# Kernel tuning notes

Hardware: AMD Instinct MI355X
Metric: run time of the kernel (lower is better)

## Reference

```python
import jax, jax.numpy as jnp
import numpy as np

N, M, D, K = 32768, 8192, 384, 9


def setup_inputs() -> dict:
    key = jax.random.key(0)
    k1, k2 = jax.random.split(key)
    return {
        "embedding": jax.random.normal(k1, (N, D), dtype=jnp.float32),
        "memory_bank": jax.random.normal(k2, (M, D), dtype=jnp.float32),
        "n_neighbors": K,
    }


def reference(embedding, memory_bank, n_neighbors):
    x_norm = jnp.sum(embedding * embedding, axis=-1, keepdims=True)      # [N, 1]
    y_norm = jnp.sum(memory_bank * memory_bank, axis=-1, keepdims=True)  # [M, 1]
    d2 = x_norm - 2.0 * jnp.matmul(embedding, memory_bank.T) + y_norm.T  # [N, M]
    dist = jnp.sqrt(jnp.maximum(d2, 0.0))
    # topk smallest along dim 1 (patch_scores, indices discarded)
    neg_top, _ = jax.lax.top_k(-dist, n_neighbors)
    patch_scores = -neg_top  # [N, K], ascending distances
    return patch_scores
```

## Files before the change

kernel.cpp:

```cpp
#include <hip/hip_runtime.h>
#include <hip/hip_bf16.h>

#define N_ROWS 32768
#define M_ROWS 8192
#define D_DIM  384
#define K_NB   9
#define BN     64
#define MHALF  (M_ROWS / 2)
#define TILES  (MHALF / BN)
#define KP     6

#define QRANGE 2048.0f
#define QSCALE (1.0f / 2048.0f)
#define QSTEPF (QRANGE / 65535.0f)
#define M2S    (-2.0f * QSCALE)
#define BIGF   3.0e38f

typedef long i64;
typedef __attribute__((ext_vector_type(2))) long i64x2;
typedef __attribute__((ext_vector_type(4))) float f32x4;
typedef __attribute__((ext_vector_type(2))) unsigned short u16x2;

__global__ __launch_bounds__(256) void FAPM_prep8(
    const float* __restrict__ emb, const float* __restrict__ mem,
    unsigned* __restrict__ A8, unsigned* __restrict__ B8,
    float* __restrict__ xn, float* __restrict__ yn) {
  const int lane = threadIdx.x & 63;
  const int row  = blockIdx.x * 4 + (threadIdx.x >> 6);
  const float* src;
  unsigned* dst;
  float* nptr;
  if (row < N_ROWS) {
    src = emb + (size_t)row * D_DIM; dst = A8 + (size_t)row * 96; nptr = xn + row;
  } else {
    int r = row - N_ROWS;
    src = mem + (size_t)r * D_DIM; dst = B8 + (size_t)r * 96; nptr = yn + r;
  }
  float s = 0.f;
  {
    int dw = lane;
    int kp = dw >> 4, r4 = dw & 15;
    int grp = r4 >> 2, half = (r4 >> 1) & 1, j = (r4 & 1) * 4;
    int k0 = kp * 64 + half * 32 + grp * 8 + j;
    f32x4 v = *(const f32x4*)(src + k0);
    s += v.x * v.x + v.y * v.y + v.z * v.z + v.w * v.w;
    int pk = __builtin_amdgcn_cvt_pk_fp8_f32(v.x, v.y, 0, false);
    pk = __builtin_amdgcn_cvt_pk_fp8_f32(v.z, v.w, pk, true);
    dst[dw] = (unsigned)pk;
  }
  if (lane < 32) {
    int dw = lane + 64;
    int kp = dw >> 4, r4 = dw & 15;
    int grp = r4 >> 2, half = (r4 >> 1) & 1, j = (r4 & 1) * 4;
    int k0 = kp * 64 + half * 32 + grp * 8 + j;
    f32x4 v = *(const f32x4*)(src + k0);
    s += v.x * v.x + v.y * v.y + v.z * v.z + v.w * v.w;
    int pk = __builtin_amdgcn_cvt_pk_fp8_f32(v.x, v.y, 0, false);
    pk = __builtin_amdgcn_cvt_pk_fp8_f32(v.z, v.w, pk, true);
    dst[dw] = (unsigned)pk;
  }
#pragma unroll
  for (int dd = 1; dd < 64; dd <<= 1) s += __shfl_xor(s, dd);
  if (lane == 0) *nptr = s;
}

__device__ __forceinline__ void merge16i(unsigned t[9], float* dst, int sub) {
  for (int s = 0; s < K_NB; ++s) {
    unsigned m  = t[0];
    int      ml = sub;
#pragma unroll
    for (int dd = 1; dd < 16; dd <<= 1) {
      unsigned ov = (unsigned)__shfl_xor((int)m, dd);
      int      ol = __shfl_xor(ml, dd);
      bool take = (ov < m) || (ov == m && ol < ml);
      m  = take ? ov : m;
      ml = take ? ol : ml;
    }
    if (sub == ml) {
#pragma unroll
      for (int j = 0; j < 8; ++j) t[j] = t[j + 1];
      t[8] = 0xFFFFu;
    }
    if (sub == 0) dst[s] = (float)m * QSTEPF;
  }
}

__global__ __launch_bounds__(256, 2) void FAPM_fused(
    const unsigned char* __restrict__ A8, const unsigned char* __restrict__ B8,
    const float* __restrict__ xn, const float* __restrict__ yn,
    float* __restrict__ part) {
  __shared__ __attribute__((aligned(128))) unsigned char As[48 * 1024];
  __shared__ __attribute__((aligned(128))) unsigned char Bs[24 * 1024];
  const int tid  = threadIdx.x;
  const int lane = tid & 63;
  const int w    = tid >> 6;
  const int sub  = lane & 15;
  const int grp  = lane >> 4;
  const int bx   = blockIdx.x;
  const int mh   = bx & 1;
  const int wrow0 = (bx >> 1) * 128 + w * 32;
  const int colbase = mh * MHALF;

  {
    const unsigned char* asrc = A8 + (size_t)(wrow0 + sub) * D_DIM + grp * 16;
#pragma unroll
    for (int rb = 0; rb < 2; ++rb)
#pragma unroll
      for (int q = 0; q < KP; ++q)
        __builtin_amdgcn_global_load_lds(
            (const __attribute__((address_space(1))) void*)(asrc + rb * 16 * D_DIM + q * 64),
            (__attribute__((address_space(3))) void*)(As + ((w * 2 + rb) * KP + q) * 1024),
            16, 0, 0);
  }
  {
    const unsigned char* bsrc =
        B8 + (size_t)(colbase + w * 16 + sub) * D_DIM + grp * 16;
#pragma unroll
    for (int q = 0; q < KP; ++q)
      __builtin_amdgcn_global_load_lds(
          (const __attribute__((address_space(1))) void*)(bsrc + q * 64),
          (__attribute__((address_space(3))) void*)(Bs + (w * KP + q) * 1024),
          16, 0, 0);
  }

  float xs0[4], xs1[4];
#pragma unroll
  for (int i = 0; i < 4; ++i) {
    xs0[i] = xn[wrow0 + grp * 4 + i] * QSCALE;
    xs1[i] = xn[wrow0 + 16 + grp * 4 + i] * QSCALE;
  }

  u16x2 tkp[4][9];
#pragma unroll
  for (int i = 0; i < 4; ++i)
#pragma unroll
    for (int j = 0; j < 9; ++j) { tkp[i][j].x = 0xFFFFu; tkp[i][j].y = 0xFFFFu; }

  const unsigned char* ar0 = As + (w * 2 + 0) * KP * 1024 + lane * 16;
  const unsigned char* ar1 = As + (w * 2 + 1) * KP * 1024 + lane * 16;
  const unsigned char* br  = Bs + lane * 16;

  asm volatile("s_waitcnt vmcnt(0)" ::: "memory");
  __syncthreads();

  for (int t = 0; t < TILES; ++t) {
    const int col0 = colbase + t * BN;
    float ysv[4];
#pragma unroll
    for (int cb = 0; cb < 4; ++cb) ysv[cb] = yn[col0 + cb * 16 + sub] * QSCALE;

    f32x4 acc[2][4];
#pragma unroll
    for (int rb = 0; rb < 2; ++rb)
#pragma unroll
      for (int cb = 0; cb < 4; ++cb) acc[rb][cb] = (f32x4){0.f, 0.f, 0.f, 0.f};

    __builtin_amdgcn_s_setprio(1);
#pragma unroll
    for (int kp = 0; kp < KP; ++kp) {
      i64x2 a0 = *(const i64x2*)(ar0 + kp * 1024);
      i64x2 a1 = *(const i64x2*)(ar1 + kp * 1024);
#pragma unroll
      for (int cb = 0; cb < 4; ++cb) {
        i64x2 b = *(const i64x2*)(br + (cb * KP + kp) * 1024);
        acc[0][cb] = __builtin_amdgcn_mfma_f32_16x16x32_fp8_fp8(a0.x, b.x, acc[0][cb], 0, 0, 0);
        acc[1][cb] = __builtin_amdgcn_mfma_f32_16x16x32_fp8_fp8(a1.x, b.x, acc[1][cb], 0, 0, 0);
        acc[0][cb] = __builtin_amdgcn_mfma_f32_16x16x32_fp8_fp8(a0.y, b.y, acc[0][cb], 0, 0, 0);
        acc[1][cb] = __builtin_amdgcn_mfma_f32_16x16x32_fp8_fp8(a1.y, b.y, acc[1][cb], 0, 0, 0);
      }
    }
    __builtin_amdgcn_s_setprio(0);
    __syncthreads();

    if (t + 1 < TILES) {
      const unsigned char* bsrc =
          B8 + (size_t)(col0 + BN + w * 16 + sub) * D_DIM + grp * 16;
#pragma unroll
      for (int q = 0; q < KP; ++q)
        __builtin_amdgcn_global_load_lds(
            (const __attribute__((address_space(1))) void*)(bsrc + q * 64),
            (__attribute__((address_space(3))) void*)(Bs + (w * KP + q) * 1024),
            16, 0, 0);
    }

#pragma unroll
    for (int cb = 0; cb < 4; ++cb) {
#pragma unroll
      for (int i = 0; i < 4; ++i) {
        float d2a = fmaf(acc[0][cb][i], M2S, xs0[i] + ysv[cb]);
        float d2b = fmaf(acc[1][cb][i], M2S, xs1[i] + ysv[cb]);
        unsigned dpu;
        asm("v_cvt_pknorm_u16_f32 %0, %1, %2" : "=v"(dpu) : "v"(d2a), "v"(d2b));
        u16x2 dp = __builtin_bit_cast(u16x2, dpu);
#pragma unroll
        for (int j = 8; j >= 1; --j)
          tkp[i][j] = __builtin_elementwise_min(
              tkp[i][j], __builtin_elementwise_max(dp, tkp[i][j - 1]));
        tkp[i][0] = __builtin_elementwise_min(tkp[i][0], dp);
      }
    }

    asm volatile("s_waitcnt vmcnt(0)" ::: "memory");
    __syncthreads();
  }

  float* pbase = part + (size_t)mh * N_ROWS * K_NB;
#pragma unroll
  for (int i = 0; i < 4; ++i) {
    unsigned ta[9], tb[9];
#pragma unroll
    for (int j = 0; j < 9; ++j) { ta[j] = tkp[i][j].x; tb[j] = tkp[i][j].y; }
    merge16i(ta, pbase + (size_t)(wrow0 + grp * 4 + i) * K_NB, sub);
    merge16i(tb, pbase + (size_t)(wrow0 + 16 + grp * 4 + i) * K_NB, sub);
  }
}

__global__ __launch_bounds__(256) void FAPM_merge(
    const float* __restrict__ part, float* __restrict__ out) {
  const int r = blockIdx.x * 256 + threadIdx.x;
  const float* pa = part + (size_t)r * K_NB;
  const float* pb = part + (size_t)N_ROWS * K_NB + (size_t)r * K_NB;
  float a[9], b[9];
#pragma unroll
  for (int j = 0; j < 9; ++j) { a[j] = pa[j]; b[j] = pb[j]; }
#pragma unroll
  for (int s = 0; s < K_NB; ++s) {
    bool ta = a[0] <= b[0];
    float m = ta ? a[0] : b[0];
    out[(size_t)r * K_NB + s] = sqrtf(fmaxf(m, 0.f));
#pragma unroll
    for (int j = 0; j < 8; ++j) {
      float an = a[j + 1], bn = b[j + 1];
      a[j] = ta ? an : a[j];
      b[j] = ta ? b[j] : bn;
    }
    a[8] = ta ? BIGF : a[8];
    b[8] = ta ? b[8] : BIGF;
  }
}

extern "C" void kernel_launch(void* const* d_in, const int* in_sizes, int n_in,
                              void* d_out, int out_size, void* d_ws, size_t ws_size,
                              hipStream_t stream) {
  const float* emb = (const float*)d_in[0];
  const float* mem = (const float*)d_in[1];
  float* out = (float*)d_out;
  char* ws = (char*)d_ws;
  size_t offA = 0;
  size_t offB = offA + (size_t)N_ROWS * D_DIM;
  size_t offX = offB + (size_t)M_ROWS * D_DIM;
  size_t offY = offX + (size_t)N_ROWS * 4;
  size_t offP = offY + (size_t)M_ROWS * 4;
  unsigned char* A8 = (unsigned char*)(ws + offA);
  unsigned char* B8 = (unsigned char*)(ws + offB);
  float* xn = (float*)(ws + offX);
  float* yn = (float*)(ws + offY);
  float* part = (float*)(ws + offP);

  FAPM_prep8<<<(N_ROWS + M_ROWS) / 4, 256, 0, stream>>>(
      emb, mem, (unsigned*)A8, (unsigned*)B8, xn, yn);
  FAPM_fused<<<(N_ROWS / 128) * 2, 256, 0, stream>>>(A8, B8, xn, yn, part);
  FAPM_merge<<<N_ROWS / 256, 256, 0, stream>>>(part, out);
}
```

Before: 225.1 us.

## Split memory bank into quarters, hold A in registers, double-buffer B tiles

```diff
diff --git a/kernel.cpp b/kernel.cpp
--- a/kernel.cpp
+++ b/kernel.cpp
@@ -6,8 +6,8 @@
 #define D_DIM  384
 #define K_NB   9
 #define BN     64
-#define MHALF  (M_ROWS / 2)
-#define TILES  (MHALF / BN)
+#define MQ     (M_ROWS / 4)
+#define TILES  (MQ / BN)
 #define KP     6
 
 #define QRANGE 2048.0f
@@ -16,9 +16,12 @@
 #define M2S    (-2.0f * QSCALE)
 #define BIGF   3.0e38f
 
+#define YS_OFF 49152
+
 typedef long i64;
 typedef __attribute__((ext_vector_type(2))) long i64x2;
 typedef __attribute__((ext_vector_type(4))) float f32x4;
+typedef __attribute__((ext_vector_type(4))) unsigned u32x4;
 typedef __attribute__((ext_vector_type(2))) unsigned short u16x2;
 
 __global__ __launch_bounds__(256) void FAPM_prep8(
@@ -85,21 +88,41 @@
   }
 }
 
-__global__ __launch_bounds__(256, 2) void FAPM_fused(
+__global__ __launch_bounds__(256, 3) void FAPM_fused(
     const unsigned char* __restrict__ A8, const unsigned char* __restrict__ B8,
     const float* __restrict__ xn, const float* __restrict__ yn,
     float* __restrict__ part) {
-  __shared__ __attribute__((aligned(128))) unsigned char As[48 * 1024];
-  __shared__ __attribute__((aligned(128))) unsigned char Bs[24 * 1024];
+  __shared__ __attribute__((aligned(128))) unsigned char LDS[53248];
   const int tid  = threadIdx.x;
   const int lane = tid & 63;
   const int w    = tid >> 6;
   const int sub  = lane & 15;
   const int grp  = lane >> 4;
   const int bx   = blockIdx.x;
-  const int mh   = bx & 1;
-  const int wrow0 = (bx >> 1) * 128 + w * 32;
-  const int colbase = mh * MHALF;
+  const int mq   = bx & 3;
+  const int wrow0 = (bx >> 2) * 128 + w * 32;
+  const int colbase = mq * MQ;
+
+  float xs0[4], xs1[4];
+#pragma unroll
+  for (int i = 0; i < 4; ++i) {
+    xs0[i] = xn[wrow0 + grp * 4 + i] * QSCALE;
+    xs1[i] = xn[wrow0 + 16 + grp * 4 + i] * QSCALE;
+  }
+
+  {
+    const float* yp = yn + colbase + tid * 8;
+    f32x4 v0 = *(const f32x4*)yp;
+    f32x4 v1 = *(const f32x4*)(yp + 4);
+    float a0 = v0.x * QSCALE, a1 = v0.y * QSCALE, a2 = v0.z * QSCALE, a3 = v0.w * QSCALE;
+    float a4 = v1.x * QSCALE, a5 = v1.y * QSCALE, a6 = v1.z * QSCALE, a7 = v1.w * QSCALE;
+    unsigned q0, q1, q2, q3;
+    asm("v_cvt_pknorm_u16_f32 %0, %1, %2" : "=v"(q0) : "v"(a0), "v"(a1));
+    asm("v_cvt_pknorm_u16_f32 %0, %1, %2" : "=v"(q1) : "v"(a2), "v"(a3));
+    asm("v_cvt_pknorm_u16_f32 %0, %1, %2" : "=v"(q2) : "v"(a4), "v"(a5));
+    asm("v_cvt_pknorm_u16_f32 %0, %1, %2" : "=v"(q3) : "v"(a6), "v"(a7));
+    *(u32x4*)(&LDS[YS_OFF + tid * 16]) = (u32x4){q0, q1, q2, q3};
+  }
 
   {
     const unsigned char* asrc = A8 + (size_t)(wrow0 + sub) * D_DIM + grp * 16;
@@ -109,45 +132,59 @@
       for (int q = 0; q < KP; ++q)
         __builtin_amdgcn_global_load_lds(
             (const __attribute__((address_space(1))) void*)(asrc + rb * 16 * D_DIM + q * 64),
-            (__attribute__((address_space(3))) void*)(As + ((w * 2 + rb) * KP + q) * 1024),
+            (__attribute__((address_space(3))) void*)(LDS + ((w * 2 + rb) * KP + q) * 1024),
             16, 0, 0);
   }
-  {
-    const unsigned char* bsrc =
-        B8 + (size_t)(colbase + w * 16 + sub) * D_DIM + grp * 16;
-#pragma unroll
-    for (int q = 0; q < KP; ++q)
-      __builtin_amdgcn_global_load_lds(
-          (const __attribute__((address_space(1))) void*)(bsrc + q * 64),
-          (__attribute__((address_space(3))) void*)(Bs + (w * KP + q) * 1024),
-          16, 0, 0);
-  }
-
-  float xs0[4], xs1[4];
-#pragma unroll
-  for (int i = 0; i < 4; ++i) {
-    xs0[i] = xn[wrow0 + grp * 4 + i] * QSCALE;
-    xs1[i] = xn[wrow0 + 16 + grp * 4 + i] * QSCALE;
-  }
-
-  u16x2 tkp[4][9];
-#pragma unroll
-  for (int i = 0; i < 4; ++i)
-#pragma unroll
-    for (int j = 0; j < 9; ++j) { tkp[i][j].x = 0xFFFFu; tkp[i][j].y = 0xFFFFu; }
-
-  const unsigned char* ar0 = As + (w * 2 + 0) * KP * 1024 + lane * 16;
-  const unsigned char* ar1 = As + (w * 2 + 1) * KP * 1024 + lane * 16;
-  const unsigned char* br  = Bs + lane * 16;
-
   asm volatile("s_waitcnt vmcnt(0)" ::: "memory");
   __syncthreads();
 
+  i64 af0[12], af1[12];
+  {
+    const unsigned char* ar0 = LDS + (w * 2) * (KP * 1024) + lane * 16;
+    const unsigned char* ar1 = ar0 + KP * 1024;
+#pragma unroll
+    for (int kp = 0; kp < KP; ++kp) {
+      i64x2 v0 = *(const i64x2*)(ar0 + kp * 1024);
+      i64x2 v1 = *(const i64x2*)(ar1 + kp * 1024);
+      af0[2 * kp] = v0.x; af0[2 * kp + 1] = v0.y;
+      af1[2 * kp] = v1.x; af1[2 * kp + 1] = v1.y;
+    }
+  }
+  __syncthreads();
+
+  const unsigned char* bsrc = B8 + (size_t)(colbase + w * 16 + sub) * D_DIM + grp * 16;
+#pragma unroll
+  for (int q = 0; q < KP; ++q)
+    __builtin_amdgcn_global_load_lds(
+        (const __attribute__((address_space(1))) void*)(bsrc + q * 64),
+        (__attribute__((address_space(3))) void*)(LDS + (w * KP + q) * 1024),
+        16, 0, 0);
+#pragma unroll
+  for (int q = 0; q < KP; ++q)
+    __builtin_amdgcn_global_load_lds(
+        (const __attribute__((address_space(1))) void*)(bsrc + 24576 + q * 64),
+        (__attribute__((address_space(3))) void*)(LDS + 24576 + (w * KP + q) * 1024),
+        16, 0, 0);
+  bsrc += 2 * 24576;
+
+  u16x2 tkp[4][9];
+#pragma unroll
+  for (int i = 0; i < 4; ++i)
+#pragma unroll
+    for (int j = 0; j < 9; ++j) { tkp[i][j].x = 0xFFFFu; tkp[i][j].y = 0xFFFFu; }
+
   for (int t = 0; t < TILES; ++t) {
-    const int col0 = colbase + t * BN;
+    const int bufo = (t & 1) * 24576;
+    if (t + 1 < TILES) asm volatile("s_waitcnt vmcnt(6)" ::: "memory");
+    else               asm volatile("s_waitcnt vmcnt(0)" ::: "memory");
+    __builtin_amdgcn_s_barrier();
+
     float ysv[4];
 #pragma unroll
-    for (int cb = 0; cb < 4; ++cb) ysv[cb] = yn[col0 + cb * 16 + sub] * QSCALE;
+    for (int cb = 0; cb < 4; ++cb) {
+      unsigned u = *(const unsigned short*)(&LDS[YS_OFF + ((t * 64 + cb * 16 + sub) << 1)]);
+      ysv[cb] = (float)u * (1.0f / 65535.0f);
+    }
 
     f32x4 acc[2][4];
 #pragma unroll
@@ -155,32 +192,30 @@
 #pragma unroll
       for (int cb = 0; cb < 4; ++cb) acc[rb][cb] = (f32x4){0.f, 0.f, 0.f, 0.f};
 
+    const unsigned char* br = LDS + bufo + lane * 16;
     __builtin_amdgcn_s_setprio(1);
 #pragma unroll
     for (int kp = 0; kp < KP; ++kp) {
-      i64x2 a0 = *(const i64x2*)(ar0 + kp * 1024);
-      i64x2 a1 = *(const i64x2*)(ar1 + kp * 1024);
 #pragma unroll
       for (int cb = 0; cb < 4; ++cb) {
         i64x2 b = *(const i64x2*)(br + (cb * KP + kp) * 1024);
-        acc[0][cb] = __builtin_amdgcn_mfma_f32_16x16x32_fp8_fp8(a0.x, b.x, acc[0][cb], 0, 0, 0);
-        acc[1][cb] = __builtin_amdgcn_mfma_f32_16x16x32_fp8_fp8(a1.x, b.x, acc[1][cb], 0, 0, 0);
-        acc[0][cb] = __builtin_amdgcn_mfma_f32_16x16x32_fp8_fp8(a0.y, b.y, acc[0][cb], 0, 0, 0);
-        acc[1][cb] = __builtin_amdgcn_mfma_f32_16x16x32_fp8_fp8(a1.y, b.y, acc[1][cb], 0, 0, 0);
+        acc[0][cb] = __builtin_amdgcn_mfma_f32_16x16x32_fp8_fp8(af0[2 * kp], b.x, acc[0][cb], 0, 0, 0);
+        acc[1][cb] = __builtin_amdgcn_mfma_f32_16x16x32_fp8_fp8(af1[2 * kp], b.x, acc[1][cb], 0, 0, 0);
+        acc[0][cb] = __builtin_amdgcn_mfma_f32_16x16x32_fp8_fp8(af0[2 * kp + 1], b.y, acc[0][cb], 0, 0, 0);
+        acc[1][cb] = __builtin_amdgcn_mfma_f32_16x16x32_fp8_fp8(af1[2 * kp + 1], b.y, acc[1][cb], 0, 0, 0);
       }
     }
     __builtin_amdgcn_s_setprio(0);
-    __syncthreads();
-
-    if (t + 1 < TILES) {
-      const unsigned char* bsrc =
-          B8 + (size_t)(col0 + BN + w * 16 + sub) * D_DIM + grp * 16;
+    __builtin_amdgcn_s_barrier();
+
+    if (t + 2 < TILES) {
 #pragma unroll
       for (int q = 0; q < KP; ++q)
         __builtin_amdgcn_global_load_lds(
             (const __attribute__((address_space(1))) void*)(bsrc + q * 64),
-            (__attribute__((address_space(3))) void*)(Bs + (w * KP + q) * 1024),
+            (__attribute__((address_space(3))) void*)(LDS + bufo + (w * KP + q) * 1024),
             16, 0, 0);
+      bsrc += 24576;
     }
 
 #pragma unroll
@@ -199,12 +234,9 @@
         tkp[i][0] = __builtin_elementwise_min(tkp[i][0], dp);
       }
     }
-
-    asm volatile("s_waitcnt vmcnt(0)" ::: "memory");
-    __syncthreads();
-  }
-
-  float* pbase = part + (size_t)mh * N_ROWS * K_NB;
+  }
+
+  float* pbase = part + (size_t)mq * N_ROWS * K_NB;
 #pragma unroll
   for (int i = 0; i < 4; ++i) {
     unsigned ta[9], tb[9];
@@ -215,27 +247,34 @@
   }
 }
 
-__global__ __launch_bounds__(256) void FAPM_merge(
+__global__ __launch_bounds__(256) void FAPM_merge4(
     const float* __restrict__ part, float* __restrict__ out) {
   const int r = blockIdx.x * 256 + threadIdx.x;
-  const float* pa = part + (size_t)r * K_NB;
-  const float* pb = part + (size_t)N_ROWS * K_NB + (size_t)r * K_NB;
-  float a[9], b[9];
-#pragma unroll
-  for (int j = 0; j < 9; ++j) { a[j] = pa[j]; b[j] = pb[j]; }
+  float l[4][9];
+#pragma unroll
+  for (int q = 0; q < 4; ++q)
+#pragma unroll
+    for (int j = 0; j < 9; ++j)
+      l[q][j] = part[(size_t)q * N_ROWS * K_NB + (size_t)r * K_NB + j];
 #pragma unroll
   for (int s = 0; s < K_NB; ++s) {
-    bool ta = a[0] <= b[0];
-    float m = ta ? a[0] : b[0];
+    float m = fminf(fminf(l[0][0], l[1][0]), fminf(l[2][0], l[3][0]));
     out[(size_t)r * K_NB + s] = sqrtf(fmaxf(m, 0.f));
+    bool t0 = (l[0][0] == m);
+    bool t1 = (l[1][0] == m) && !t0;
+    bool t2 = (l[2][0] == m) && !t0 && !t1;
+    bool t3 = !(t0 || t1 || t2);
 #pragma unroll
     for (int j = 0; j < 8; ++j) {
-      float an = a[j + 1], bn = b[j + 1];
-      a[j] = ta ? an : a[j];
-      b[j] = ta ? b[j] : bn;
-    }
-    a[8] = ta ? BIGF : a[8];
-    b[8] = ta ? b[8] : BIGF;
+      l[0][j] = t0 ? l[0][j + 1] : l[0][j];
+      l[1][j] = t1 ? l[1][j + 1] : l[1][j];
+      l[2][j] = t2 ? l[2][j + 1] : l[2][j];
+      l[3][j] = t3 ? l[3][j + 1] : l[3][j];
+    }
+    l[0][8] = t0 ? BIGF : l[0][8];
+    l[1][8] = t1 ? BIGF : l[1][8];
+    l[2][8] = t2 ? BIGF : l[2][8];
+    l[3][8] = t3 ? BIGF : l[3][8];
   }
 }
 
@@ -259,6 +298,6 @@
 
   FAPM_prep8<<<(N_ROWS + M_ROWS) / 4, 256, 0, stream>>>(
       emb, mem, (unsigned*)A8, (unsigned*)B8, xn, yn);
-  FAPM_fused<<<(N_ROWS / 128) * 2, 256, 0, stream>>>(A8, B8, xn, yn, part);
-  FAPM_merge<<<N_ROWS / 256, 256, 0, stream>>>(part, out);
-}
+  FAPM_fused<<<(N_ROWS / 128) * 4, 256, 0, stream>>>(A8, B8, xn, yn, part);
+  FAPM_merge4<<<N_ROWS / 256, 256, 0, stream>>>(part, out);
+}
```

New measurement: 210.6 us. 1.07x faster.
